# Kernel tuning notes

Hardware: AMD Instinct MI355X
Metric: run time of the kernel (lower is better)

Reference implementation:

```python
import jax, jax.numpy as jnp
import numpy as np


def _wkv_scan(key, value, time_decay, time_first):
    # Numerically-stabilized RWKV WKV recurrence; key/value: [B,T,C]
    w = -jnp.exp(time_decay)  # [C]
    B, T, C = key.shape

    def step(carry, kv):
        num, den, mx = carry
        k, v = kv  # [B,C] each
        # output at this timestep
        mo = jnp.maximum(mx, k + time_first)
        e1 = jnp.exp(mx - mo)
        e2 = jnp.exp(k + time_first - mo)
        out = (e1 * num + e2 * v) / (e1 * den + e2)
        # state update
        ms = jnp.maximum(mx + w, k)
        e1s = jnp.exp(mx + w - ms)
        e2s = jnp.exp(k - ms)
        return (e1s * num + e2s * v, e1s * den + e2s, ms), out

    init = (jnp.zeros((B, C), key.dtype),
            jnp.zeros((B, C), key.dtype),
            jnp.full((B, C), -1e38, key.dtype))
    kT = jnp.swapaxes(key, 0, 1)   # [T,B,C]
    vT = jnp.swapaxes(value, 0, 1)
    _, outs = jax.lax.scan(step, init, (kT, vT))
    return jnp.swapaxes(outs, 0, 1)  # [B,T,C]


def setup_inputs() -> dict:
    key = jax.random.key(0)
    ks = jax.random.split(key, 10)
    B, T, C = 8, 2048, 1024
    s = 1.0 / np.sqrt(C)
    return {
        "x": jax.random.normal(ks[0], (B, T, C), jnp.float32),
        "wk": jax.random.normal(ks[1], (C, C), jnp.float32) * s,
        "wv": jax.random.normal(ks[2], (C, C), jnp.float32) * s,
        "wr": jax.random.normal(ks[3], (C, C), jnp.float32) * s,
        "wo": jax.random.normal(ks[4], (C, C), jnp.float32) * s,
        "time_decay": jax.random.normal(ks[5], (C,), jnp.float32) * 0.5,
        "time_first": jax.random.normal(ks[6], (C,), jnp.float32) * 0.5,
        "mix_k": jax.random.uniform(ks[7], (1, 1, C), jnp.float32),
        "mix_v": jax.random.uniform(ks[8], (1, 1, C), jnp.float32),
        "mix_r": jax.random.uniform(ks[9], (1, 1, C), jnp.float32),
    }


def reference(x, wk, wv, wr, wo, time_decay, time_first, mix_k, mix_v, mix_r):
    # time_shift: prev_x[:,0]=0, prev_x[:,t]=x[:,t-1]  (ZeroPad2d((0,0,1,-1)))
    prev_x = jnp.pad(x, ((0, 0), (1, 0), (0, 0)))[:, :-1, :]
    k_in = x * mix_k + prev_x * (1.0 - mix_k)
    v_in = x * mix_v + prev_x * (1.0 - mix_v)
    r_in = x * mix_r + prev_x * (1.0 - mix_r)
    key = jnp.einsum('btc,dc->btd', k_in, wk)
    value = jnp.einsum('btc,dc->btd', v_in, wv)
    receptance = jax.nn.sigmoid(jnp.einsum('btc,dc->btd', r_in, wr))
    wkv = _wkv_scan(key, value, time_decay, time_first)
    rwkv = receptance * wkv
    return jnp.einsum('btc,dc->btd', rwkv, wo)
```

## Files before the change

kernel.cpp:

```cpp
#include <hip/hip_runtime.h>
#include <stdint.h>


using bf16x8 = __attribute__((ext_vector_type(8))) __bf16;
using f32x4  = __attribute__((ext_vector_type(4))) float;

union FU { float f; unsigned int u; };

__device__ __forceinline__ unsigned short f2b(float f) {
  FU v; v.f = f;
  unsigned int u = v.u;
  return (unsigned short)((u + 0x7fffu + ((u >> 16) & 1u)) >> 16);
}
__device__ __forceinline__ float b2f(unsigned short h) {
  FU v; v.u = ((unsigned int)h) << 16; return v.f;
}

__device__ __forceinline__ void gl_lds16(const unsigned short* g,
                                         const unsigned short* l) {
  __builtin_amdgcn_global_load_lds(
      (const __attribute__((address_space(1))) void*)g,
      (__attribute__((address_space(3))) void*)l, 16, 0, 0);
}

__global__ __launch_bounds__(256) void prep_kernel(
    const float* __restrict__ x,
    const float* __restrict__ w0, const float* __restrict__ w1,
    const float* __restrict__ w2, const float* __restrict__ w3,
    unsigned short* __restrict__ o0, unsigned short* __restrict__ o1,
    unsigned short* __restrict__ o2, unsigned short* __restrict__ o3,
    const float* __restrict__ mk, const float* __restrict__ mv,
    const float* __restrict__ mr,
    unsigned short* __restrict__ ok, unsigned short* __restrict__ ov,
    unsigned short* __restrict__ orr, int T, int C)
{
  int bid = blockIdx.x;
  if (bid < 4096) {
    int mat = bid >> 10, blk = bid & 1023;
    const float* src = (mat == 0) ? w0 : (mat == 1) ? w1 : (mat == 2) ? w2 : w3;
    unsigned short* dst = (mat == 0) ? o0 : (mat == 1) ? o1 : (mat == 2) ? o2 : o3;
    int i = blk * 1024 + threadIdx.x * 4;
    float4 v = *(const float4*)(src + i);
    union { int2 i2; unsigned short u[4]; } o;
    o.u[0] = f2b(v.x); o.u[1] = f2b(v.y); o.u[2] = f2b(v.z); o.u[3] = f2b(v.w);
    *(int2*)(dst + i) = o.i2;
    return;
  }
  int i = (bid - 4096) * 256 + threadIdx.x;
  int base = i * 8;
  int row = base / C;
  int t = row - (row / T) * T;
  int c = base - row * C;
  float xv[8], pv[8];
  *(float4*)&xv[0] = *(const float4*)(x + base);
  *(float4*)&xv[4] = *(const float4*)(x + base + 4);
  if (t > 0) {
    *(float4*)&pv[0] = *(const float4*)(x + base - C);
    *(float4*)&pv[4] = *(const float4*)(x + base - C + 4);
  } else {
#pragma unroll
    for (int e = 0; e < 8; ++e) pv[e] = 0.f;
  }
  float mkv[8], mvv[8], mrv[8];
  *(float4*)&mkv[0] = *(const float4*)(mk + c);
  *(float4*)&mkv[4] = *(const float4*)(mk + c + 4);
  *(float4*)&mvv[0] = *(const float4*)(mv + c);
  *(float4*)&mvv[4] = *(const float4*)(mv + c + 4);
  *(float4*)&mrv[0] = *(const float4*)(mr + c);
  *(float4*)&mrv[4] = *(const float4*)(mr + c + 4);
  union { int4 i4; unsigned short u[8]; } a, b2, d;
#pragma unroll
  for (int e = 0; e < 8; ++e) {
    float xe = xv[e], pe = pv[e];
    a.u[e]  = f2b(xe * mkv[e] + pe * (1.f - mkv[e]));
    b2.u[e] = f2b(xe * mvv[e] + pe * (1.f - mvv[e]));
    d.u[e]  = f2b(xe * mrv[e] + pe * (1.f - mrv[e]));
  }
  *(int4*)(ok + base)  = a.i4;
  *(int4*)(ov + base)  = b2.i4;
  *(int4*)(orr + base) = d.i4;
}

template<typename EPI>
__device__ __forceinline__ void gemm_core(
    const unsigned short* __restrict__ A,
    const unsigned short* __restrict__ W,
    int mBlk, int nBlk, int N, int K, EPI epi)
{
  __shared__ __align__(16) unsigned short As[128 * 32];
  __shared__ __align__(16) unsigned short Bs[128 * 32];
  const int tid  = threadIdx.x;
  const int lane = tid & 63;
  const int w    = tid >> 6;
  const int wm   = w >> 1, wn = w & 1;
  const int col  = lane & 15, quad = lane >> 4;

  const int s0 = 2 * w, s1 = 2 * w + 1;
  const int rA0 = s0 * 16 + (lane >> 2), rA1 = s1 * 16 + (lane >> 2);
  const int kc  = (lane & 3) * 8;

  const f32x4 zero = {0.f, 0.f, 0.f, 0.f};
  f32x4 acc[4][4];
#pragma unroll
  for (int i = 0; i < 4; ++i)
#pragma unroll
    for (int j = 0; j < 4; ++j) acc[i][j] = zero;

  const unsigned short* Ab = A + (size_t)mBlk * K;
  const unsigned short* Wb = W + (size_t)nBlk * K;
  const unsigned short* gA0 = Ab + (size_t)rA0 * K + kc;
  const unsigned short* gA1 = Ab + (size_t)rA1 * K + kc;
  const unsigned short* gB0 = Wb + (size_t)rA0 * K + kc;
  const unsigned short* gB1 = Wb + (size_t)rA1 * K + kc;
  const unsigned short* lA0 = &As[s0 * 512];
  const unsigned short* lA1 = &As[s1 * 512];
  const unsigned short* lB0 = &Bs[s0 * 512];
  const unsigned short* lB1 = &Bs[s1 * 512];

  for (int k0 = 0; k0 < K; k0 += 32) {
    gl_lds16(gA0 + k0, lA0);
    gl_lds16(gA1 + k0, lA1);
    gl_lds16(gB0 + k0, lB0);
    gl_lds16(gB1 + k0, lB1);
    __syncthreads();

    bf16x8 af[4], bg[4];
#pragma unroll
    for (int i = 0; i < 4; ++i)
      af[i] = *(const bf16x8*)&As[(wm * 64 + i * 16 + col) * 32 + quad * 8];
#pragma unroll
    for (int j = 0; j < 4; ++j)
      bg[j] = *(const bf16x8*)&Bs[(wn * 64 + j * 16 + col) * 32 + quad * 8];
#pragma unroll
    for (int i = 0; i < 4; ++i)
#pragma unroll
      for (int j = 0; j < 4; ++j)
        acc[i][j] = __builtin_amdgcn_mfma_f32_16x16x32_bf16(af[i], bg[j], acc[i][j], 0, 0, 0);

    __syncthreads();
  }

  const int mBase = mBlk + wm * 64, nBase = nBlk + wn * 64;
#pragma unroll
  for (int i = 0; i < 4; ++i)
#pragma unroll
    for (int j = 0; j < 4; ++j)
#pragma unroll
      for (int r = 0; r < 4; ++r)
        epi(mBase + i * 16 + quad * 4 + r, nBase + j * 16 + col, acc[i][j][r]);
}

__global__ __launch_bounds__(256) void gemmKV_kernel(
    const unsigned short* __restrict__ A0, const unsigned short* __restrict__ A1,
    const unsigned short* __restrict__ W0, const unsigned short* __restrict__ W1,
    unsigned short* __restrict__ out0, unsigned short* __restrict__ out1,
    int N, int K)
{
  int z = blockIdx.z;
  const unsigned short* A = (z == 0) ? A0 : A1;
  const unsigned short* W = (z == 0) ? W0 : W1;
  unsigned short* out = (z == 0) ? out0 : out1;
  gemm_core(A, W, blockIdx.x * 128, blockIdx.y * 128, N, K,
            [&](int rg, int cg, float v) {
              out[(size_t)rg * N + cg] = f2b(v);
            });
}

__global__ __launch_bounds__(256) void gemmR_kernel(
    const unsigned short* __restrict__ A, const unsigned short* __restrict__ W,
    unsigned short* __restrict__ out, int N, int K)
{
  gemm_core(A, W, blockIdx.x * 128, blockIdx.y * 128, N, K,
            [&](int rg, int cg, float v) {
              float s = 1.0f / (1.0f + __expf(-v));
              out[(size_t)rg * N + cg] = f2b(s);
            });
}

__global__ __launch_bounds__(256) void gemmO_kernel(
    const unsigned short* __restrict__ A, const unsigned short* __restrict__ W,
    float* __restrict__ out, int N, int K)
{
  gemm_core(A, W, blockIdx.x * 128, blockIdx.y * 128, N, K,
            [&](int rg, int cg, float v) {
              out[(size_t)rg * N + cg] = v;
            });
}

__global__ __launch_bounds__(256) void wkv_pass1(
    const unsigned short* __restrict__ kb, const unsigned short* __restrict__ vb,
    const float* __restrict__ td,
    float* __restrict__ snum, float* __restrict__ sden, float* __restrict__ smx,
    int T, int C, int L)
{
  int g = blockIdx.x * 256 + threadIdx.x;
  int bc = g & 8191;
  int ch = g >> 13;
  int c = bc & 1023;
  float w = -__expf(td[c]);
  float num = 0.f, den = 0.f, mx = -1e38f;
  size_t base = ((size_t)(bc >> 10) * T + (size_t)ch * L) * C + c;
  for (int j0 = 0; j0 < L; j0 += 8) {
    float kq[8], vq[8];
#pragma unroll
    for (int j = 0; j < 8; ++j) {
      size_t a = base + (size_t)(j0 + j) * C;
      kq[j] = b2f(kb[a]);
      vq[j] = b2f(vb[a]);
    }
#pragma unroll
    for (int j = 0; j < 8; ++j) {
      float k = kq[j], v = vq[j];
      float mw = mx + w;
      float ms = fmaxf(mw, k);
      float s1 = __expf(mw - ms);
      float s2 = __expf(k - ms);
      num = s1 * num + s2 * v;
      den = s1 * den + s2;
      mx = ms;
    }
  }
  int idx = ch * 8192 + bc;
  snum[idx] = num; sden[idx] = den; smx[idx] = mx;
}

__global__ __launch_bounds__(64) void wkv_pass2(
    const float* __restrict__ snum, const float* __restrict__ sden,
    const float* __restrict__ smx, const float* __restrict__ td,
    float* __restrict__ inum, float* __restrict__ iden, float* __restrict__ imx,
    int L)
{
  int bc = blockIdx.x * 64 + threadIdx.x;
  int c = bc & 1023;
  float Wl = -__expf(td[c]) * (float)L;
  float num = 0.f, den = 0.f, mx = -1e38f;
#pragma unroll
  for (int ch = 0; ch < 32; ++ch) {
    int idx = ch * 8192 + bc;
    inum[idx] = num; iden[idx] = den; imx[idx] = mx;
    float sn = snum[idx], sd = sden[idx], sm = smx[idx];
    float mi = mx + Wl;
    float mo = fmaxf(mi, sm);
    float e1 = __expf(mi - mo);
    float e2 = __expf(sm - mo);
    num = e1 * num + e2 * sn;
    den = e1 * den + e2 * sd;
    mx = mo;
  }
}

__global__ __launch_bounds__(256) void wkv_pass3(
    const unsigned short* __restrict__ kb, const unsigned short* __restrict__ vb,
    const unsigned short* __restrict__ rsig,
    const float* __restrict__ td, const float* __restrict__ tf,
    const float* __restrict__ inum, const float* __restrict__ iden,
    const float* __restrict__ imx,
    unsigned short* __restrict__ rwkv, int T, int C, int L)
{
  int g = blockIdx.x * 256 + threadIdx.x;
  int bc = g & 8191;
  int ch = g >> 13;
  int c = bc & 1023;
  float w = -__expf(td[c]);
  float u = tf[c];
  int idx = ch * 8192 + bc;
  float num = inum[idx], den = iden[idx], mx = imx[idx];
  size_t base = ((size_t)(bc >> 10) * T + (size_t)ch * L) * C + c;
  for (int j0 = 0; j0 < L; j0 += 8) {
    float kq[8], vq[8], rq[8];
#pragma unroll
    for (int j = 0; j < 8; ++j) {
      size_t a = base + (size_t)(j0 + j) * C;
      kq[j] = b2f(kb[a]);
      vq[j] = b2f(vb[a]);
      rq[j] = b2f(rsig[a]);
    }
#pragma unroll
    for (int j = 0; j < 8; ++j) {
      float k = kq[j], v = vq[j];
      float ku = k + u;
      float mo = fmaxf(mx, ku);
      float e1 = __expf(mx - mo);
      float e2 = __expf(ku - mo);
      float o = (e1 * num + e2 * v) / (e1 * den + e2);
      rwkv[base + (size_t)(j0 + j) * C] = f2b(rq[j] * o);
      float mw = mx + w;
      float ms = fmaxf(mw, k);
      float s1 = __expf(mw - ms);
      float s2 = __expf(k - ms);
      num = s1 * num + s2 * v;
      den = s1 * den + s2;
      mx = ms;
    }
  }
}

extern "C" void kernel_launch(void* const* d_in, const int* in_sizes, int n_in,
                              void* d_out, int out_size, void* d_ws, size_t ws_size,
                              hipStream_t stream)
{
  const float* x  = (const float*)d_in[0];
  const float* wk = (const float*)d_in[1];
  const float* wv = (const float*)d_in[2];
  const float* wr = (const float*)d_in[3];
  const float* wo = (const float*)d_in[4];
  const float* td = (const float*)d_in[5];
  const float* tf = (const float*)d_in[6];
  const float* mk = (const float*)d_in[7];
  const float* mv = (const float*)d_in[8];
  const float* mr = (const float*)d_in[9];

  const int B = 8, T = 2048, C = 1024;
  const int M = B * T;
  const int NC = 32, L = 64;
  const size_t MB = 1024 * 1024;

  char* ws = (char*)d_ws;
  unsigned short* bufK = (unsigned short*)(ws);
  unsigned short* bufV = (unsigned short*)(ws + 32 * MB);
  unsigned short* bufR = (unsigned short*)(ws + 64 * MB);
  unsigned short* kb   = (unsigned short*)(ws + 96 * MB);
  unsigned short* wkb  = (unsigned short*)(ws + 128 * MB);
  unsigned short* wvb  = (unsigned short*)(ws + 130 * MB);
  unsigned short* wrb  = (unsigned short*)(ws + 132 * MB);
  unsigned short* wob  = (unsigned short*)(ws + 134 * MB);
  float* snum = (float*)(ws + 136 * MB);
  float* sden = (float*)(ws + 137 * MB);
  float* smx  = (float*)(ws + 138 * MB);
  float* inum = (float*)(ws + 139 * MB);
  float* iden = (float*)(ws + 140 * MB);
  float* imx  = (float*)(ws + 141 * MB);
  unsigned short* vb   = (unsigned short*)(ws + 142 * MB);
  unsigned short* rsig = bufV;
  unsigned short* rwkv = bufR;

  dim3 gGemm(M / 128, C / 128);
  dim3 gGemmKV(M / 128, C / 128, 2);
  int scanBlocks = (B * C * NC) / 256;

  prep_kernel<<<12288, 256, 0, stream>>>(x, wk, wv, wr, wo, wkb, wvb, wrb, wob,
                                         mk, mv, mr, bufK, bufV, bufR, T, C);
  gemmKV_kernel<<<gGemmKV, 256, 0, stream>>>(bufK, bufV, wkb, wvb, kb, vb, C, C);
  gemmR_kernel<<<gGemm, 256, 0, stream>>>(bufR, wrb, rsig, C, C);
  wkv_pass1<<<scanBlocks, 256, 0, stream>>>(kb, vb, td, snum, sden, smx, T, C, L);
  wkv_pass2<<<(B * C) / 64, 64, 0, stream>>>(snum, sden, smx, td, inum, iden, imx, L);
  wkv_pass3<<<scanBlocks, 256, 0, stream>>>(kb, vb, rsig, td, tf, inum, iden, imx,
                                            rwkv, T, C, L);
  gemmO_kernel<<<gGemm, 256, 0, stream>>>(rwkv, wob, (float*)d_out, C, C);
}
```

Measured before the change: 397.5 us.

## Replace GEMM core with 256x256 double-buffered, swizzled, pipelined MFMA kernel

Replaces the simple 128x128 single-buffered GEMM with a 256x256 tile, 512-thread kernel. It double-buffers LDS with 64-wide K tiles and XOR-swizzles the LDS layout. Staging of the next tiles is interleaved inside the MFMA quarters, using manual barriers, waitcnt and setprio. The goal is to hide global-load latency, cut LDS bank conflicts and raise arithmetic intensity. K=1024 is now hardcoded, and the large LDS footprint with 512 threads may limit occupancy.

```diff
diff --git a/kernel.cpp b/kernel.cpp
--- a/kernel.cpp
+++ b/kernel.cpp
@@ -22,6 +22,11 @@
       (const __attribute__((address_space(1))) void*)g,
       (__attribute__((address_space(3))) void*)l, 16, 0, 0);
 }
+
+#define SBAR()  asm volatile("s_barrier" ::: "memory")
+#define LGKM0() do { asm volatile("s_waitcnt lgkmcnt(0)" ::: "memory"); \
+                     __builtin_amdgcn_sched_barrier(0); } while (0)
+#define VMW(n)  asm volatile("s_waitcnt vmcnt(" #n ")" ::: "memory")
 
 __global__ __launch_bounds__(256) void prep_kernel(
     const float* __restrict__ x,
@@ -81,110 +86,195 @@
   *(int4*)(orr + base) = d.i4;
 }
 
+
+__device__ __forceinline__ void stageHalf(
+    const unsigned short* __restrict__ g,
+    const unsigned short* l,
+    int rh, int kt, int w, int rl, int koffel)
+{
+#pragma unroll
+  for (int c = 0; c < 2; ++c) {
+    int rows = rh * 128 + (2 * w + c) * 8;
+    gl_lds16(g + (size_t)(rows + rl) * 1024 + kt * 64 + koffel,
+             l + rows * 64);
+  }
+}
+
+template<int Q>
+__device__ __forceinline__ void quadMfma(f32x4 (&acc)[8][4],
+    bf16x8 a00, bf16x8 a01, bf16x8 a10, bf16x8 a11, bf16x8 (&b)[4][2])
+{
+#pragma unroll
+  for (int j = 0; j < 4; ++j) {
+    acc[2*Q][j]   = __builtin_amdgcn_mfma_f32_16x16x32_bf16(a00, b[j][0], acc[2*Q][j],   0, 0, 0);
+    acc[2*Q][j]   = __builtin_amdgcn_mfma_f32_16x16x32_bf16(a01, b[j][1], acc[2*Q][j],   0, 0, 0);
+    acc[2*Q+1][j] = __builtin_amdgcn_mfma_f32_16x16x32_bf16(a10, b[j][0], acc[2*Q+1][j], 0, 0, 0);
+    acc[2*Q+1][j] = __builtin_amdgcn_mfma_f32_16x16x32_bf16(a11, b[j][1], acc[2*Q+1][j], 0, 0, 0);
+  }
+}
+
+template<bool ST_A, bool ST_B, int VMN>
+__device__ __forceinline__ void ktile(
+    const unsigned short* aR, const unsigned short* bR,
+    const unsigned short* aW, const unsigned short* bW,
+    const unsigned short* Am, const unsigned short* Wn,
+    int ktA, int ktB, int w, int wm, int wn, int col, int quad,
+    int swzel, int rl, int koffel, f32x4 (&acc)[8][4])
+{
+  const int ks0 = (quad * 8) ^ swzel;
+  const int ks1 = (32 + quad * 8) ^ swzel;
+  bf16x8 b[4][2];
+#pragma unroll
+  for (int j = 0; j < 4; ++j) {
+    const unsigned short* br = bR + (wn * 64 + j * 16 + col) * 64;
+    b[j][0] = *(const bf16x8*)(br + ks0);
+    b[j][1] = *(const bf16x8*)(br + ks1);
+  }
+  const unsigned short* ar = aR + (wm * 128 + col) * 64;
+  {
+    bf16x8 a00 = *(const bf16x8*)(ar + 0 * 1024 + ks0);
+    bf16x8 a01 = *(const bf16x8*)(ar + 0 * 1024 + ks1);
+    bf16x8 a10 = *(const bf16x8*)(ar + 1 * 1024 + ks0);
+    bf16x8 a11 = *(const bf16x8*)(ar + 1 * 1024 + ks1);
+    if (ST_A) stageHalf(Am, aW, 0, ktA, w, rl, koffel);
+    SBAR(); LGKM0();
+    __builtin_amdgcn_s_setprio(1);
+    quadMfma<0>(acc, a00, a01, a10, a11, b);
+    __builtin_amdgcn_s_setprio(0);
+    SBAR();
+  }
+  {
+    bf16x8 a00 = *(const bf16x8*)(ar + 2 * 1024 + ks0);
+    bf16x8 a01 = *(const bf16x8*)(ar + 2 * 1024 + ks1);
+    bf16x8 a10 = *(const bf16x8*)(ar + 3 * 1024 + ks0);
+    bf16x8 a11 = *(const bf16x8*)(ar + 3 * 1024 + ks1);
+    if (ST_A) stageHalf(Am, aW, 1, ktA, w, rl, koffel);
+    SBAR(); LGKM0();
+    __builtin_amdgcn_s_setprio(1);
+    quadMfma<1>(acc, a00, a01, a10, a11, b);
+    __builtin_amdgcn_s_setprio(0);
+    SBAR();
+  }
+  {
+    bf16x8 a00 = *(const bf16x8*)(ar + 4 * 1024 + ks0);
+    bf16x8 a01 = *(const bf16x8*)(ar + 4 * 1024 + ks1);
+    bf16x8 a10 = *(const bf16x8*)(ar + 5 * 1024 + ks0);
+    bf16x8 a11 = *(const bf16x8*)(ar + 5 * 1024 + ks1);
+    if (ST_B) stageHalf(Wn, bW, 0, ktB, w, rl, koffel);
+    SBAR(); LGKM0();
+    __builtin_amdgcn_s_setprio(1);
+    quadMfma<2>(acc, a00, a01, a10, a11, b);
+    __builtin_amdgcn_s_setprio(0);
+    SBAR();
+  }
+  {
+    bf16x8 a00 = *(const bf16x8*)(ar + 6 * 1024 + ks0);
+    bf16x8 a01 = *(const bf16x8*)(ar + 6 * 1024 + ks1);
+    bf16x8 a10 = *(const bf16x8*)(ar + 7 * 1024 + ks0);
+    bf16x8 a11 = *(const bf16x8*)(ar + 7 * 1024 + ks1);
+    if (ST_B) stageHalf(Wn, bW, 1, ktB, w, rl, koffel);
+    SBAR(); LGKM0();
+    __builtin_amdgcn_s_setprio(1);
+    quadMfma<3>(acc, a00, a01, a10, a11, b);
+    __builtin_amdgcn_s_setprio(0);
+    if constexpr (VMN == 4) { VMW(4); }
+    else if constexpr (VMN == 0) { VMW(0); }
+    SBAR();
+  }
+}
+
 template<typename EPI>
-__device__ __forceinline__ void gemm_core(
+__device__ __forceinline__ void gemm256(
     const unsigned short* __restrict__ A,
     const unsigned short* __restrict__ W,
-    int mBlk, int nBlk, int N, int K, EPI epi)
-{
-  __shared__ __align__(16) unsigned short As[128 * 32];
-  __shared__ __align__(16) unsigned short Bs[128 * 32];
+    EPI epi)
+{
+  __shared__ __align__(16) unsigned short As[2][256 * 64];
+  __shared__ __align__(16) unsigned short Bs[2][256 * 64];
   const int tid  = threadIdx.x;
   const int lane = tid & 63;
   const int w    = tid >> 6;
-  const int wm   = w >> 1, wn = w & 1;
+  const int wm   = w >> 2, wn = w & 3;
   const int col  = lane & 15, quad = lane >> 4;
-
-  const int s0 = 2 * w, s1 = 2 * w + 1;
-  const int rA0 = s0 * 16 + (lane >> 2), rA1 = s1 * 16 + (lane >> 2);
-  const int kc  = (lane & 3) * 8;
-
-  const f32x4 zero = {0.f, 0.f, 0.f, 0.f};
-  f32x4 acc[4][4];
-#pragma unroll
-  for (int i = 0; i < 4; ++i)
-#pragma unroll
-    for (int j = 0; j < 4; ++j) acc[i][j] = zero;
-
-  const unsigned short* Ab = A + (size_t)mBlk * K;
-  const unsigned short* Wb = W + (size_t)nBlk * K;
-  const unsigned short* gA0 = Ab + (size_t)rA0 * K + kc;
-  const unsigned short* gA1 = Ab + (size_t)rA1 * K + kc;
-  const unsigned short* gB0 = Wb + (size_t)rA0 * K + kc;
-  const unsigned short* gB1 = Wb + (size_t)rA1 * K + kc;
-  const unsigned short* lA0 = &As[s0 * 512];
-  const unsigned short* lA1 = &As[s1 * 512];
-  const unsigned short* lB0 = &Bs[s0 * 512];
-  const unsigned short* lB1 = &Bs[s1 * 512];
-
-  for (int k0 = 0; k0 < K; k0 += 32) {
-    gl_lds16(gA0 + k0, lA0);
-    gl_lds16(gA1 + k0, lA1);
-    gl_lds16(gB0 + k0, lB0);
-    gl_lds16(gB1 + k0, lB1);
-    __syncthreads();
-
-    bf16x8 af[4], bg[4];
-#pragma unroll
-    for (int i = 0; i < 4; ++i)
-      af[i] = *(const bf16x8*)&As[(wm * 64 + i * 16 + col) * 32 + quad * 8];
+  const int swzel  = (lane & 7) << 3;
+  const int rl     = lane >> 3;
+  const int koffel = ((lane & 7) ^ rl) << 3;
+  const int mBase = blockIdx.x * 256;
+  const int nBase = blockIdx.y * 256;
+  const unsigned short* Am = A + (size_t)mBase * 1024;
+  const unsigned short* Wn = W + (size_t)nBase * 1024;
+
+  f32x4 acc[8][4];
+  const f32x4 z = {0.f, 0.f, 0.f, 0.f};
+#pragma unroll
+  for (int i = 0; i < 8; ++i)
+#pragma unroll
+    for (int j = 0; j < 4; ++j) acc[i][j] = z;
+
+  stageHalf(Wn, &Bs[0][0], 0, 0, w, rl, koffel);
+  stageHalf(Wn, &Bs[0][0], 1, 0, w, rl, koffel);
+  stageHalf(Am, &As[0][0], 0, 0, w, rl, koffel);
+  stageHalf(Am, &As[0][0], 1, 0, w, rl, koffel);
+  stageHalf(Wn, &Bs[1][0], 0, 1, w, rl, koffel);
+  stageHalf(Wn, &Bs[1][0], 1, 1, w, rl, koffel);
+  VMW(4); SBAR();
+
+#pragma unroll
+  for (int t = 0; t < 14; t += 2) {
+    ktile<true, true, 4>(&As[0][0], &Bs[0][0], &As[1][0], &Bs[0][0],
+                         Am, Wn, t + 1, t + 2,
+                         w, wm, wn, col, quad, swzel, rl, koffel, acc);
+    ktile<true, true, 4>(&As[1][0], &Bs[1][0], &As[0][0], &Bs[1][0],
+                         Am, Wn, t + 2, t + 3,
+                         w, wm, wn, col, quad, swzel, rl, koffel, acc);
+  }
+  ktile<true, false, 0>(&As[0][0], &Bs[0][0], &As[1][0], &Bs[0][0],
+                        Am, Wn, 15, 0,
+                        w, wm, wn, col, quad, swzel, rl, koffel, acc);
+  ktile<false, false, -1>(&As[1][0], &Bs[1][0], &As[0][0], &Bs[1][0],
+                          Am, Wn, 0, 0,
+                          w, wm, wn, col, quad, swzel, rl, koffel, acc);
+
+  const int mB = mBase + wm * 128, nB = nBase + wn * 64;
+#pragma unroll
+  for (int i = 0; i < 8; ++i)
 #pragma unroll
     for (int j = 0; j < 4; ++j)
-      bg[j] = *(const bf16x8*)&Bs[(wn * 64 + j * 16 + col) * 32 + quad * 8];
-#pragma unroll
-    for (int i = 0; i < 4; ++i)
-#pragma unroll
-      for (int j = 0; j < 4; ++j)
-        acc[i][j] = __builtin_amdgcn_mfma_f32_16x16x32_bf16(af[i], bg[j], acc[i][j], 0, 0, 0);
-
-    __syncthreads();
-  }
-
-  const int mBase = mBlk + wm * 64, nBase = nBlk + wn * 64;
-#pragma unroll
-  for (int i = 0; i < 4; ++i)
-#pragma unroll
-    for (int j = 0; j < 4; ++j)
 #pragma unroll
       for (int r = 0; r < 4; ++r)
-        epi(mBase + i * 16 + quad * 4 + r, nBase + j * 16 + col, acc[i][j][r]);
-}
-
-__global__ __launch_bounds__(256) void gemmKV_kernel(
+        epi(mB + i * 16 + quad * 4 + r, nB + j * 16 + col, acc[i][j][r]);
+}
+
+__global__ __launch_bounds__(512, 2) void gemmKV2_kernel(
     const unsigned short* __restrict__ A0, const unsigned short* __restrict__ A1,
     const unsigned short* __restrict__ W0, const unsigned short* __restrict__ W1,
-    unsigned short* __restrict__ out0, unsigned short* __restrict__ out1,
-    int N, int K)
-{
-  int z = blockIdx.z;
-  const unsigned short* A = (z == 0) ? A0 : A1;
-  const unsigned short* W = (z == 0) ? W0 : W1;
-  unsigned short* out = (z == 0) ? out0 : out1;
-  gemm_core(A, W, blockIdx.x * 128, blockIdx.y * 128, N, K,
-            [&](int rg, int cg, float v) {
-              out[(size_t)rg * N + cg] = f2b(v);
-            });
-}
-
-__global__ __launch_bounds__(256) void gemmR_kernel(
+    unsigned short* __restrict__ out0, unsigned short* __restrict__ out1)
+{
+  const int z = blockIdx.z;
+  const unsigned short* A = z ? A1 : A0;
+  const unsigned short* W = z ? W1 : W0;
+  unsigned short* out = z ? out1 : out0;
+  gemm256(A, W, [&](int r, int c, float v) {
+    out[(size_t)r * 1024 + c] = f2b(v);
+  });
+}
+
+__global__ __launch_bounds__(512, 2) void gemmR2_kernel(
     const unsigned short* __restrict__ A, const unsigned short* __restrict__ W,
-    unsigned short* __restrict__ out, int N, int K)
-{
-  gemm_core(A, W, blockIdx.x * 128, blockIdx.y * 128, N, K,
-            [&](int rg, int cg, float v) {
-              float s = 1.0f / (1.0f + __expf(-v));
-              out[(size_t)rg * N + cg] = f2b(s);
-            });
-}
-
-__global__ __launch_bounds__(256) void gemmO_kernel(
+    unsigned short* __restrict__ out)
+{
+  gemm256(A, W, [&](int r, int c, float v) {
+    out[(size_t)r * 1024 + c] = f2b(1.0f / (1.0f + __expf(-v)));
+  });
+}
+
+__global__ __launch_bounds__(512, 2) void gemmO2_kernel(
     const unsigned short* __restrict__ A, const unsigned short* __restrict__ W,
-    float* __restrict__ out, int N, int K)
-{
-  gemm_core(A, W, blockIdx.x * 128, blockIdx.y * 128, N, K,
-            [&](int rg, int cg, float v) {
-              out[(size_t)rg * N + cg] = v;
-            });
+    float* __restrict__ out)
+{
+  gemm256(A, W, [&](int r, int c, float v) {
+    out[(size_t)r * 1024 + c] = v;
+  });
 }
 
 __global__ __launch_bounds__(256) void wkv_pass1(
@@ -334,17 +424,17 @@
   unsigned short* rsig = bufV;
   unsigned short* rwkv = bufR;
 
-  dim3 gGemm(M / 128, C / 128);
-  dim3 gGemmKV(M / 128, C / 128, 2);
+  dim3 gKV(M / 256, C / 256, 2);
+  dim3 gG(M / 256, C / 256);
   int scanBlocks = (B * C * NC) / 256;
 
   prep_kernel<<<12288, 256, 0, stream>>>(x, wk, wv, wr, wo, wkb, wvb, wrb, wob,
                                          mk, mv, mr, bufK, bufV, bufR, T, C);
-  gemmKV_kernel<<<gGemmKV, 256, 0, stream>>>(bufK, bufV, wkb, wvb, kb, vb, C, C);
-  gemmR_kernel<<<gGemm, 256, 0, stream>>>(bufR, wrb, rsig, C, C);
+  gemmKV2_kernel<<<gKV, 512, 0, stream>>>(bufK, bufV, wkb, wvb, kb, vb);
+  gemmR2_kernel<<<gG, 512, 0, stream>>>(bufR, wrb, rsig);
   wkv_pass1<<<scanBlocks, 256, 0, stream>>>(kb, vb, td, snum, sden, smx, T, C, L);
   wkv_pass2<<<(B * C) / 64, 64, 0, stream>>>(snum, sden, smx, td, inum, iden, imx, L);
   wkv_pass3<<<scanBlocks, 256, 0, stream>>>(kb, vb, rsig, td, tf, inum, iden, imx,
                                             rwkv, T, C, L);
-  gemmO_kernel<<<gGemm, 256, 0, stream>>>(rwkv, wob, (float*)d_out, C, C);
-}
+  gemmO2_kernel<<<gG, 512, 0, stream>>>(rwkv, wob, (float*)d_out);
+}
```

New measurement: 414.3 us. +4.2%, slower.
